# Optimization experiments

Measured on AMD Instinct MI355X. Metric: run time of the kernel, lower is better.

## Reference

```python
import jax, jax.numpy as jnp
import numpy as np

B, S, E, H, FF = 8, 1024, 1024, 16, 4096
DK = E // H
EPS = 1.1920929e-07  # torch RMSNorm default eps = finfo(float32).eps


def _rmsnorm(x, g):
    return x * jax.lax.rsqrt(jnp.mean(x * x, axis=-1, keepdims=True) + EPS) * g


def _rope(q, k):
    # q, k: [B, H, S, DK]; standard rotate-half RoPE, theta=10000
    d = q.shape[-1]
    s = q.shape[-2]
    inv_freq = 1.0 / (10000.0 ** (jnp.arange(0, d, 2, dtype=jnp.float32) / d))
    ang = jnp.arange(s, dtype=jnp.float32)[:, None] * inv_freq  # [S, d/2]
    cos = jnp.concatenate([jnp.cos(ang), jnp.cos(ang)], axis=-1)  # [S, d]
    sin = jnp.concatenate([jnp.sin(ang), jnp.sin(ang)], axis=-1)

    def rot(x):
        x1, x2 = jnp.split(x, 2, axis=-1)
        return jnp.concatenate([-x2, x1], axis=-1)

    return q * cos + rot(q) * sin, k * cos + rot(k) * sin


def setup_inputs() -> dict:
    key = jax.random.key(0)
    ks = jax.random.split(key, 16)
    sc = 0.02
    inp = {
        "x": jax.random.normal(ks[0], (B, S, E), dtype=jnp.float32),
        "WQ": jax.random.normal(ks[1], (E, E), dtype=jnp.float32) * sc,
        "bQ": jnp.zeros((E,), jnp.float32),
        "WK": jax.random.normal(ks[2], (E, E), dtype=jnp.float32) * sc,
        "bK": jnp.zeros((E,), jnp.float32),
        "WV": jax.random.normal(ks[3], (E, E), dtype=jnp.float32) * sc,
        "bV": jnp.zeros((E,), jnp.float32),
        "WO": jax.random.normal(ks[4], (E, E), dtype=jnp.float32) * sc,
        "bO": jnp.zeros((E,), jnp.float32),
        "W1": jax.random.normal(ks[5], (E, FF), dtype=jnp.float32) * sc,
        "b1": jnp.zeros((FF,), jnp.float32),
        "W2": jax.random.normal(ks[6], (FF, E), dtype=jnp.float32) * sc,
        "b2": jnp.zeros((E,), jnp.float32),
        "g1": jnp.ones((E,), jnp.float32),
        "g2": jnp.ones((E,), jnp.float32),
    }
    return inp


def reference(x, WQ, bQ, WK, bK, WV, bV, WO, bO, W1, b1, W2, b2, g1, g2):
    b, s, e = x.shape

    def attn(h):
        q = (h @ WQ + bQ).reshape(b, s, H, DK).transpose(0, 2, 1, 3)
        k = (h @ WK + bK).reshape(b, s, H, DK).transpose(0, 2, 1, 3)
        v = (h @ WV + bV).reshape(b, s, H, DK).transpose(0, 2, 1, 3)
        q, k = _rope(q, k)
        scores = jnp.einsum("bhqd,bhkd->bhqk", q, k) / jnp.sqrt(jnp.float32(DK))
        p = jax.nn.softmax(scores, axis=-1)
        o = jnp.einsum("bhqk,bhkd->bhqd", p, v)
        o = o.transpose(0, 2, 1, 3).reshape(b, s, e)
        return o @ WO + bO

    def ffn(h):
        return jax.nn.relu(h @ W1 + b1) @ W2 + b2

    x = x + attn(_rmsnorm(x, g1))
    x = x + ffn(_rmsnorm(x, g2))
    return x
```

## Files before the change

### kernel.cpp

```cpp
#include <hip/hip_runtime.h>
#include <math.h>

#define B_ 8
#define S_ 1024
#define E_ 1024
#define H_ 16
#define FF_ 4096

typedef __attribute__((ext_vector_type(8))) short bf16x8;
typedef __attribute__((ext_vector_type(4))) float f32x4;

__device__ __forceinline__ unsigned short f2bf(float f) {
  union { float f; unsigned u; } v;
  v.f = f;
  unsigned r = v.u + 0x7fffu + ((v.u >> 16) & 1u);
  return (unsigned short)(r >> 16);
}
__device__ __forceinline__ float bf2f(unsigned short u) {
  union { unsigned u; float f; } v;
  v.u = ((unsigned)u) << 16;
  return v.f;
}
__device__ __forceinline__ unsigned fbits(float f) {
  union { float f; unsigned u; } v;
  v.f = f;
  return v.u;
}

__device__ __forceinline__ void glds16(const void* g, void* l) {
  __builtin_amdgcn_global_load_lds(
      (const __attribute__((address_space(1))) unsigned int*)g,
      (__attribute__((address_space(3))) unsigned int*)l, 16, 0, 0);
}

__global__ __launch_bounds__(256) void wconvT(const float* __restrict__ W,
                                              unsigned short* __restrict__ Wt,
                                              int K, int N) {
  __shared__ float t[32][33];
  const int tx = threadIdx.x & 31, ty = threadIdx.x >> 5;
  const int n0 = blockIdx.x * 32, k0 = blockIdx.y * 32;
#pragma unroll
  for (int p = 0; p < 4; ++p)
    t[ty + p * 8][tx] = W[(size_t)(k0 + ty + p * 8) * N + n0 + tx];
  __syncthreads();
#pragma unroll
  for (int p = 0; p < 4; ++p)
    Wt[(size_t)(n0 + ty + p * 8) * K + k0 + tx] = f2bf(t[tx][ty + p * 8]);
}

__global__ __launch_bounds__(256) void bpack(const float* __restrict__ bQ,
                                             const float* __restrict__ bK,
                                             const float* __restrict__ bV,
                                             float* __restrict__ o) {
  const int i = blockIdx.x * 256 + threadIdx.x;
  const float v = (i < 1024) ? bQ[i] : ((i < 2048) ? bK[i - 1024] : bV[i - 2048]);
  o[i] = v;
}

__global__ __launch_bounds__(256) void rmsnorm_kernel(const float* __restrict__ x,
                                                      const float* __restrict__ g,
                                                      unsigned short* __restrict__ out) {
  const int row = blockIdx.x;
  const int t = threadIdx.x;
  const float4 v = ((const float4*)(x + (size_t)row * E_))[t];
  float ss = v.x * v.x + v.y * v.y + v.z * v.z + v.w * v.w;
#pragma unroll
  for (int off = 32; off > 0; off >>= 1) ss += __shfl_down(ss, off);
  __shared__ float sred[4];
  if ((t & 63) == 0) sred[t >> 6] = ss;
  __syncthreads();
  const float tot = sred[0] + sred[1] + sred[2] + sred[3];
  const float rinv = rsqrtf(tot * (1.0f / E_) + 1.1920929e-07f);
  const float4 gv = ((const float4*)g)[t];
  ushort4 o;
  o.x = f2bf(v.x * rinv * gv.x);
  o.y = f2bf(v.y * rinv * gv.y);
  o.z = f2bf(v.z * rinv * gv.z);
  o.w = f2bf(v.w * rinv * gv.w);
  ((ushort4*)(out + (size_t)row * E_))[t] = o;
}

template <int OUT_BF16, int RELU, int RES>
__global__ __launch_bounds__(256) void gemm_bf16(const unsigned short* __restrict__ A,
                                                 const unsigned short* __restrict__ Bt,
                                                 const float* __restrict__ bias,
                                                 const float* __restrict__ res,
                                                 void* __restrict__ C,
                                                 int M, int N, int K) {
  __shared__ unsigned short As[128 * 32];
  __shared__ unsigned short Bs[128 * 32];
  const int tid = threadIdx.x;
  const int w = tid >> 6;
  const int lane = tid & 63;

  const int nb = gridDim.x;
  const int id = blockIdx.x;
  const int lid = (id & 7) * (nb >> 3) + (id >> 3);
  const int per = (M >> 7) * 8;
  const int grp = lid / per;
  const int rem = lid - grp * per;
  const int bn = (grp * 8 + (rem & 7)) * 128;
  const int bm = (rem >> 3) * 128;

  const int wm = (w & 1) * 64, wn = (w >> 1) * 64;

  f32x4 acc[4][4];
#pragma unroll
  for (int i = 0; i < 4; ++i)
#pragma unroll
    for (int j = 0; j < 4; ++j) acc[i][j] = (f32x4){0.f, 0.f, 0.f, 0.f};

  const unsigned short* Ap0 = A + (size_t)(bm + w * 32 + (lane >> 2)) * K + (lane & 3) * 8;
  const unsigned short* Ap1 = Ap0 + (size_t)16 * K;
  const unsigned short* Bp0 = Bt + (size_t)(bn + w * 32 + (lane >> 2)) * K + (lane & 3) * 8;
  const unsigned short* Bp1 = Bp0 + (size_t)16 * K;
  unsigned short* AsD0 = &As[w * 1024];
  unsigned short* AsD1 = AsD0 + 512;
  unsigned short* BsD0 = &Bs[w * 1024];
  unsigned short* BsD1 = BsD0 + 512;

  const int fr = lane & 15;
  const int fk = (lane >> 4) * 8;

  for (int k0 = 0; k0 < K; k0 += 32) {
    __syncthreads();
    glds16(Ap0 + k0, AsD0);
    glds16(Ap1 + k0, AsD1);
    glds16(Bp0 + k0, BsD0);
    glds16(Bp1 + k0, BsD1);
    __syncthreads();
    bf16x8 a[4], b[4];
#pragma unroll
    for (int im = 0; im < 4; ++im)
      a[im] = *(const bf16x8*)&As[(wm + im * 16 + fr) * 32 + fk];
#pragma unroll
    for (int in = 0; in < 4; ++in)
      b[in] = *(const bf16x8*)&Bs[(wn + in * 16 + fr) * 32 + fk];
#pragma unroll
    for (int im = 0; im < 4; ++im)
#pragma unroll
      for (int in = 0; in < 4; ++in)
        acc[im][in] = __builtin_amdgcn_mfma_f32_16x16x32_bf16(a[im], b[in], acc[im][in], 0, 0, 0);
  }

#pragma unroll
  for (int im = 0; im < 4; ++im) {
    const int row0 = bm + wm + im * 16 + (lane >> 4) * 4;
#pragma unroll
    for (int in = 0; in < 4; ++in) {
      const int col = bn + wn + in * 16 + (lane & 15);
      const float bv = bias[col];
#pragma unroll
      for (int r = 0; r < 4; ++r) {
        float v = acc[im][in][r] + bv;
        if (RES) v += res[(size_t)(row0 + r) * N + col];
        if (RELU) v = fmaxf(v, 0.0f);
        if (OUT_BF16)
          ((unsigned short*)C)[(size_t)(row0 + r) * N + col] = f2bf(v);
        else
          ((float*)C)[(size_t)(row0 + r) * N + col] = v;
      }
    }
  }
}

#define QSCALE 0.1803368801111f
__global__ __launch_bounds__(256) void rope_kernel(unsigned short* __restrict__ QKV) {
  const int i = blockIdx.x * 256 + threadIdx.x;
  const int fi = i & 31;
  const int h = (i >> 5) & 15;
  const int bs = i >> 9;
  const int s = bs & (S_ - 1);
  const float inv = exp2f(-0.4152410118f * (float)fi);
  const float ang = (float)s * inv;
  const float cs = __cosf(ang), sn = __sinf(ang);
  const size_t base = (size_t)bs * 3072 + h * 64 + fi;
  const float q1 = bf2f(QKV[base]), q2 = bf2f(QKV[base + 32]);
  QKV[base] = f2bf((q1 * cs - q2 * sn) * QSCALE);
  QKV[base + 32] = f2bf((q2 * cs + q1 * sn) * QSCALE);
  const size_t kb = base + 1024;
  const float k1 = bf2f(QKV[kb]), k2 = bf2f(QKV[kb + 32]);
  QKV[kb] = f2bf(k1 * cs - k2 * sn);
  QKV[kb + 32] = f2bf(k2 * cs + k1 * sn);
}

__global__ __launch_bounds__(256) void vtrans(const unsigned short* __restrict__ QKV,
                                              unsigned short* __restrict__ Vt) {
  __shared__ unsigned short T[64 * 66];
  const int tid = threadIdx.x;
  const int st = blockIdx.x, bh = blockIdx.y;
  const int b = bh >> 4, h = bh & 15;
  const int sx = tid & 15, sy = tid >> 4;
#pragma unroll
  for (int p = 0; p < 4; ++p) {
    const int sl = p * 16 + sy;
    const ushort4 v = *(const ushort4*)&QKV[(size_t)(b * S_ + st * 64 + sl) * 3072 + 2048 + h * 64 + sx * 4];
    *(ushort4*)&T[sl * 66 + sx * 4] = v;
  }
  __syncthreads();
#pragma unroll
  for (int p = 0; p < 4; ++p) {
    const int dl = p * 16 + sy;
    ushort4 o;
    o.x = T[(sx * 4 + 0) * 66 + dl];
    o.y = T[(sx * 4 + 1) * 66 + dl];
    o.z = T[(sx * 4 + 2) * 66 + dl];
    o.w = T[(sx * 4 + 3) * 66 + dl];
    *(ushort4*)&Vt[(size_t)(bh * 64 + dl) * S_ + st * 64 + sx * 4] = o;
  }
}

__global__ __launch_bounds__(256) void attn_v3(const unsigned short* __restrict__ QKV,
                                               const unsigned short* __restrict__ Vt,
                                               unsigned short* __restrict__ Og) {
  __shared__ unsigned short Kf[8 * 512];
  __shared__ unsigned short Vf[8 * 512];
  __shared__ unsigned short Ps[4][32 * 72];
  const int tid = threadIdx.x;
  const int w = tid >> 6, lane = tid & 63;
  const int qt = blockIdx.x, bh = blockIdx.y;
  const int b = bh >> 4, h = bh & 15;
  const int fr = lane & 15, g = lane >> 4, fk = g * 8;
  const int q0w = qt * 128 + w * 32;

  bf16x8 qB[2][2];
#pragma unroll
  for (int nt = 0; nt < 2; ++nt)
#pragma unroll
    for (int c = 0; c < 2; ++c)
      qB[nt][c] = *(const bf16x8*)&QKV[(size_t)(b * S_ + q0w + nt * 16 + fr) * 3072 +
                                       h * 64 + c * 32 + fk];

  f32x4 o[4][2];
#pragma unroll
  for (int mt = 0; mt < 4; ++mt)
#pragma unroll
    for (int nt = 0; nt < 2; ++nt) o[mt][nt] = (f32x4){0.f, 0.f, 0.f, 0.f};
  float l[2] = {0.0f, 0.0f};

  for (int kt = 0; kt < 16; ++kt) {
    __syncthreads();
#pragma unroll
    for (int p = 0; p < 4; ++p) {
      const int u = w * 4 + p;
      if (u < 8) {
        const int mt = u >> 1, c = u & 1;
        glds16(QKV + (size_t)(b * S_ + kt * 64 + mt * 16 + fr) * 3072 +
                   1024 + h * 64 + c * 32 + fk,
               &Kf[u * 512]);
      } else {
        const int v = u - 8, mt = v >> 1, c = v & 1;
        glds16(Vt + (size_t)(bh * 64 + mt * 16 + fr) * S_ + kt * 64 + c * 32 + fk,
               &Vf[v * 512]);
      }
    }
    __syncthreads();

    f32x4 s[4][2];
#pragma unroll
    for (int mt = 0; mt < 4; ++mt) {
      const bf16x8 k0 = *(const bf16x8*)&Kf[(mt * 2 + 0) * 512 + lane * 8];
      const bf16x8 k1 = *(const bf16x8*)&Kf[(mt * 2 + 1) * 512 + lane * 8];
#pragma unroll
      for (int nt = 0; nt < 2; ++nt) {
        f32x4 a = (f32x4){0.f, 0.f, 0.f, 0.f};
        a = __builtin_amdgcn_mfma_f32_16x16x32_bf16(k0, qB[nt][0], a, 0, 0, 0);
        a = __builtin_amdgcn_mfma_f32_16x16x32_bf16(k1, qB[nt][1], a, 0, 0, 0);
        s[mt][nt] = a;
      }
    }

#pragma unroll
    for (int nt = 0; nt < 2; ++nt) {
      float rs = 0.0f;
#pragma unroll
      for (int mt = 0; mt < 4; ++mt)
#pragma unroll
        for (int r = 0; r < 4; ++r) {
          const float p = exp2f(s[mt][nt][r]);
          s[mt][nt][r] = p;
          rs += p;
        }
      rs += __shfl_xor(rs, 16);
      rs += __shfl_xor(rs, 32);
      l[nt] += rs;
    }

#pragma unroll
    for (int nt = 0; nt < 2; ++nt)
#pragma unroll
      for (int mt = 0; mt < 4; ++mt) {
        uint2 pk;
        pk.x = __builtin_amdgcn_perm(fbits(s[mt][nt][1]), fbits(s[mt][nt][0]), 0x07060302u);
        pk.y = __builtin_amdgcn_perm(fbits(s[mt][nt][3]), fbits(s[mt][nt][2]), 0x07060302u);
        *(uint2*)&Ps[w][(nt * 16 + fr) * 72 + mt * 16 + g * 4] = pk;
      }

    bf16x8 pB[2][2];
#pragma unroll
    for (int nt = 0; nt < 2; ++nt)
#pragma unroll
      for (int c = 0; c < 2; ++c)
        pB[nt][c] = *(const bf16x8*)&Ps[w][(nt * 16 + fr) * 72 + c * 32 + fk];
#pragma unroll
    for (int mt = 0; mt < 4; ++mt) {
      const bf16x8 v0 = *(const bf16x8*)&Vf[(mt * 2 + 0) * 512 + lane * 8];
      const bf16x8 v1 = *(const bf16x8*)&Vf[(mt * 2 + 1) * 512 + lane * 8];
#pragma unroll
      for (int nt = 0; nt < 2; ++nt) {
        o[mt][nt] = __builtin_amdgcn_mfma_f32_16x16x32_bf16(v0, pB[nt][0], o[mt][nt], 0, 0, 0);
        o[mt][nt] = __builtin_amdgcn_mfma_f32_16x16x32_bf16(v1, pB[nt][1], o[mt][nt], 0, 0, 0);
      }
    }
  }

  __syncthreads();
  const float linv0 = 1.0f / l[0], linv1 = 1.0f / l[1];
#pragma unroll
  for (int nt = 0; nt < 2; ++nt) {
    const float li = nt ? linv1 : linv0;
#pragma unroll
    for (int mt = 0; mt < 4; ++mt) {
      uint2 pk;
      pk.x = __builtin_amdgcn_perm(fbits(o[mt][nt][1] * li), fbits(o[mt][nt][0] * li), 0x07060302u);
      pk.y = __builtin_amdgcn_perm(fbits(o[mt][nt][3] * li), fbits(o[mt][nt][2] * li), 0x07060302u);
      *(uint2*)&Ps[w][(nt * 16 + fr) * 72 + mt * 16 + g * 4] = pk;
    }
  }
  __syncthreads();
  const int qr = lane >> 1, hf = lane & 1;
#pragma unroll
  for (int c = 0; c < 2; ++c) {
    const bf16x8 vv = *(const bf16x8*)&Ps[w][qr * 72 + hf * 16 + c * 32];
    *(bf16x8*)&Og[(size_t)(b * S_ + q0w + qr) * E_ + h * 64 + hf * 16 + c * 32] = vv;
  }
}

extern "C" void kernel_launch(void* const* d_in, const int* in_sizes, int n_in,
                              void* d_out, int out_size, void* d_ws, size_t ws_size,
                              hipStream_t stream) {
  const float* x  = (const float*)d_in[0];
  const float* WQ = (const float*)d_in[1];
  const float* bQ = (const float*)d_in[2];
  const float* WK = (const float*)d_in[3];
  const float* bK = (const float*)d_in[4];
  const float* WV = (const float*)d_in[5];
  const float* bV = (const float*)d_in[6];
  const float* WO = (const float*)d_in[7];
  const float* bO = (const float*)d_in[8];
  const float* W1 = (const float*)d_in[9];
  const float* b1 = (const float*)d_in[10];
  const float* W2 = (const float*)d_in[11];
  const float* b2 = (const float*)d_in[12];
  const float* g1 = (const float*)d_in[13];
  const float* g2 = (const float*)d_in[14];
  float* out = (float*)d_out;

  char* ws = (char*)d_ws;
  const size_t MB = 1024 * 1024;
  unsigned short* h1   = (unsigned short*)(ws + 0 * MB);
  unsigned short* QKV  = (unsigned short*)(ws + 16 * MB);
  unsigned short* Vt   = (unsigned short*)(ws + 64 * MB);
  unsigned short* Ob   = (unsigned short*)(ws + 80 * MB);
  float*          x1   = (float*)(ws + 96 * MB);
  unsigned short* h2   = (unsigned short*)(ws + 128 * MB);
  unsigned short* mid  = (unsigned short*)(ws + 16 * MB);
  unsigned short* WQKVt= (unsigned short*)(ws + 144 * MB);
  unsigned short* WOt  = (unsigned short*)(ws + 150 * MB);
  unsigned short* W1t  = (unsigned short*)(ws + 152 * MB);
  unsigned short* W2t  = (unsigned short*)(ws + 160 * MB);
  float*          bqkv = (float*)(ws + 168 * MB);

  const int M = B_ * S_;

  wconvT<<<dim3(32, 32), 256, 0, stream>>>(WQ, WQKVt, E_, E_);
  wconvT<<<dim3(32, 32), 256, 0, stream>>>(WK, WQKVt + 1024 * 1024, E_, E_);
  wconvT<<<dim3(32, 32), 256, 0, stream>>>(WV, WQKVt + 2 * 1024 * 1024, E_, E_);
  wconvT<<<dim3(32, 32), 256, 0, stream>>>(WO, WOt, E_, E_);
  wconvT<<<dim3(128, 32), 256, 0, stream>>>(W1, W1t, E_, FF_);
  wconvT<<<dim3(32, 128), 256, 0, stream>>>(W2, W2t, FF_, E_);
  bpack<<<12, 256, 0, stream>>>(bQ, bK, bV, bqkv);

  rmsnorm_kernel<<<M, 256, 0, stream>>>(x, g1, h1);

  gemm_bf16<1, 0, 0><<<24 * 64, 256, 0, stream>>>(h1, WQKVt, bqkv, nullptr, QKV, M, 3072, E_);

  rope_kernel<<<(B_ * S_ * H_ * 32) / 256, 256, 0, stream>>>(QKV);

  vtrans<<<dim3(16, 128), 256, 0, stream>>>(QKV, Vt);

  attn_v3<<<dim3(8, B_ * H_), 256, 0, stream>>>(QKV, Vt, Ob);

  gemm_bf16<0, 0, 1><<<8 * 64, 256, 0, stream>>>(Ob, WOt, bO, x, x1, M, E_, E_);

  rmsnorm_kernel<<<M, 256, 0, stream>>>(x1, g2, h2);

  gemm_bf16<1, 1, 0><<<32 * 64, 256, 0, stream>>>(h2, W1t, b1, nullptr, mid, M, FF_, E_);

  gemm_bf16<0, 0, 1><<<8 * 64, 256, 0, stream>>>(mid, W2t, b2, x1, out, M, E_, FF_);
}
```

Before: 549.9 us.

## Fuse RoPE and V transpose into QKV GEMM, double-buffer attention, use N64 GEMM

The QKV projection GEMM now applies RoPE and the Q scale in its epilogue and writes V already transposed. This removes the separate rope and vtrans kernels and their extra global round trips. Attention gets double-buffered K/V shared-memory staging so the next tile's loads overlap compute, and some syncs are removed. The N=1024 output GEMMs (WO, W2) switch to a 128x64 tile kernel that launches 1024 blocks, raising occupancy and CU coverage. The risks are strided scalar stores in the QKV epilogue and a possible shared-memory race now that the barriers are gone.

```diff
diff --git a/kernel.cpp b/kernel.cpp
--- a/kernel.cpp
+++ b/kernel.cpp
@@ -9,6 +9,9 @@
 
 typedef __attribute__((ext_vector_type(8))) short bf16x8;
 typedef __attribute__((ext_vector_type(4))) float f32x4;
+
+#define QSCALE 0.1803368801111f
+#define LG2_10K 0.4152410118f
 
 __device__ __forceinline__ unsigned short f2bf(float f) {
   union { float f; unsigned u; } v;
@@ -164,57 +167,202 @@
   }
 }
 
-#define QSCALE 0.1803368801111f
-__global__ __launch_bounds__(256) void rope_kernel(unsigned short* __restrict__ QKV) {
-  const int i = blockIdx.x * 256 + threadIdx.x;
-  const int fi = i & 31;
-  const int h = (i >> 5) & 15;
-  const int bs = i >> 9;
-  const int s = bs & (S_ - 1);
-  const float inv = exp2f(-0.4152410118f * (float)fi);
-  const float ang = (float)s * inv;
-  const float cs = __cosf(ang), sn = __sinf(ang);
-  const size_t base = (size_t)bs * 3072 + h * 64 + fi;
-  const float q1 = bf2f(QKV[base]), q2 = bf2f(QKV[base + 32]);
-  QKV[base] = f2bf((q1 * cs - q2 * sn) * QSCALE);
-  QKV[base + 32] = f2bf((q2 * cs + q1 * sn) * QSCALE);
-  const size_t kb = base + 1024;
-  const float k1 = bf2f(QKV[kb]), k2 = bf2f(QKV[kb + 32]);
-  QKV[kb] = f2bf(k1 * cs - k2 * sn);
-  QKV[kb + 32] = f2bf(k2 * cs + k1 * sn);
-}
-
-__global__ __launch_bounds__(256) void vtrans(const unsigned short* __restrict__ QKV,
-                                              unsigned short* __restrict__ Vt) {
-  __shared__ unsigned short T[64 * 66];
+template <int OUT_BF16, int RELU, int RES>
+__global__ __launch_bounds__(256) void gemm_n64(const unsigned short* __restrict__ A,
+                                                const unsigned short* __restrict__ Bt,
+                                                const float* __restrict__ bias,
+                                                const float* __restrict__ res,
+                                                void* __restrict__ C,
+                                                int M, int N, int K) {
+  __shared__ unsigned short As[128 * 32];
+  __shared__ unsigned short Bs[64 * 32];
   const int tid = threadIdx.x;
-  const int st = blockIdx.x, bh = blockIdx.y;
-  const int b = bh >> 4, h = bh & 15;
-  const int sx = tid & 15, sy = tid >> 4;
-#pragma unroll
-  for (int p = 0; p < 4; ++p) {
-    const int sl = p * 16 + sy;
-    const ushort4 v = *(const ushort4*)&QKV[(size_t)(b * S_ + st * 64 + sl) * 3072 + 2048 + h * 64 + sx * 4];
-    *(ushort4*)&T[sl * 66 + sx * 4] = v;
-  }
-  __syncthreads();
-#pragma unroll
-  for (int p = 0; p < 4; ++p) {
-    const int dl = p * 16 + sy;
-    ushort4 o;
-    o.x = T[(sx * 4 + 0) * 66 + dl];
-    o.y = T[(sx * 4 + 1) * 66 + dl];
-    o.z = T[(sx * 4 + 2) * 66 + dl];
-    o.w = T[(sx * 4 + 3) * 66 + dl];
-    *(ushort4*)&Vt[(size_t)(bh * 64 + dl) * S_ + st * 64 + sx * 4] = o;
-  }
-}
-
-__global__ __launch_bounds__(256) void attn_v3(const unsigned short* __restrict__ QKV,
+  const int w = tid >> 6;
+  const int lane = tid & 63;
+
+  const int nbn = N >> 6;
+  const int bm = (blockIdx.x / nbn) * 128;
+  const int bn = (blockIdx.x % nbn) * 64;
+
+  const int wm = (w & 1) * 64, wn = (w >> 1) * 32;
+
+  f32x4 acc[4][2];
+#pragma unroll
+  for (int i = 0; i < 4; ++i)
+#pragma unroll
+    for (int j = 0; j < 2; ++j) acc[i][j] = (f32x4){0.f, 0.f, 0.f, 0.f};
+
+  const unsigned short* Ap0 = A + (size_t)(bm + w * 32 + (lane >> 2)) * K + (lane & 3) * 8;
+  const unsigned short* Ap1 = Ap0 + (size_t)16 * K;
+  const unsigned short* Bp0 = Bt + (size_t)(bn + w * 16 + (lane >> 2)) * K + (lane & 3) * 8;
+  unsigned short* AsD0 = &As[w * 1024];
+  unsigned short* AsD1 = AsD0 + 512;
+  unsigned short* BsD0 = &Bs[w * 512];
+
+  const int fr = lane & 15;
+  const int fk = (lane >> 4) * 8;
+
+  for (int k0 = 0; k0 < K; k0 += 32) {
+    __syncthreads();
+    glds16(Ap0 + k0, AsD0);
+    glds16(Ap1 + k0, AsD1);
+    glds16(Bp0 + k0, BsD0);
+    __syncthreads();
+    bf16x8 a[4], b[2];
+#pragma unroll
+    for (int im = 0; im < 4; ++im)
+      a[im] = *(const bf16x8*)&As[(wm + im * 16 + fr) * 32 + fk];
+#pragma unroll
+    for (int in = 0; in < 2; ++in)
+      b[in] = *(const bf16x8*)&Bs[(wn + in * 16 + fr) * 32 + fk];
+#pragma unroll
+    for (int im = 0; im < 4; ++im)
+#pragma unroll
+      for (int in = 0; in < 2; ++in)
+        acc[im][in] = __builtin_amdgcn_mfma_f32_16x16x32_bf16(a[im], b[in], acc[im][in], 0, 0, 0);
+  }
+
+#pragma unroll
+  for (int im = 0; im < 4; ++im) {
+    const int row0 = bm + wm + im * 16 + (lane >> 4) * 4;
+#pragma unroll
+    for (int in = 0; in < 2; ++in) {
+      const int col = bn + wn + in * 16 + fr;
+      const float bv = bias[col];
+#pragma unroll
+      for (int r = 0; r < 4; ++r) {
+        float v = acc[im][in][r] + bv;
+        if (RES) v += res[(size_t)(row0 + r) * N + col];
+        if (RELU) v = fmaxf(v, 0.0f);
+        if (OUT_BF16)
+          ((unsigned short*)C)[(size_t)(row0 + r) * N + col] = f2bf(v);
+        else
+          ((float*)C)[(size_t)(row0 + r) * N + col] = v;
+      }
+    }
+  }
+}
+
+__global__ __launch_bounds__(256) void gemm_qkv(const unsigned short* __restrict__ A,
+                                                const unsigned short* __restrict__ Bt,
+                                                const float* __restrict__ bias,
+                                                unsigned short* __restrict__ QKV,
+                                                unsigned short* __restrict__ Vt,
+                                                int M, int K) {
+  const int N = 3072;
+  __shared__ unsigned short As[128 * 32];
+  __shared__ unsigned short Bs[128 * 32];
+  const int tid = threadIdx.x;
+  const int w = tid >> 6;
+  const int lane = tid & 63;
+
+  const int nb = gridDim.x;
+  const int id = blockIdx.x;
+  const int lid = (id & 7) * (nb >> 3) + (id >> 3);
+  const int per = (M >> 7) * 8;
+  const int grp = lid / per;
+  const int rem = lid - grp * per;
+  const int bn = (grp * 8 + (rem & 7)) * 128;
+  const int bm = (rem >> 3) * 128;
+
+  const int wm = (w & 1) * 64, wn = (w >> 1) * 64;
+
+  f32x4 acc[4][4];
+#pragma unroll
+  for (int i = 0; i < 4; ++i)
+#pragma unroll
+    for (int j = 0; j < 4; ++j) acc[i][j] = (f32x4){0.f, 0.f, 0.f, 0.f};
+
+  const unsigned short* Ap0 = A + (size_t)(bm + w * 32 + (lane >> 2)) * K + (lane & 3) * 8;
+  const unsigned short* Ap1 = Ap0 + (size_t)16 * K;
+  const unsigned short* Bp0 = Bt + (size_t)(bn + w * 32 + (lane >> 2)) * K + (lane & 3) * 8;
+  const unsigned short* Bp1 = Bp0 + (size_t)16 * K;
+  unsigned short* AsD0 = &As[w * 1024];
+  unsigned short* AsD1 = AsD0 + 512;
+  unsigned short* BsD0 = &Bs[w * 1024];
+  unsigned short* BsD1 = BsD0 + 512;
+
+  const int fr = lane & 15;
+  const int fk = (lane >> 4) * 8;
+
+  for (int k0 = 0; k0 < K; k0 += 32) {
+    __syncthreads();
+    glds16(Ap0 + k0, AsD0);
+    glds16(Ap1 + k0, AsD1);
+    glds16(Bp0 + k0, BsD0);
+    glds16(Bp1 + k0, BsD1);
+    __syncthreads();
+    bf16x8 a[4], b[4];
+#pragma unroll
+    for (int im = 0; im < 4; ++im)
+      a[im] = *(const bf16x8*)&As[(wm + im * 16 + fr) * 32 + fk];
+#pragma unroll
+    for (int in = 0; in < 4; ++in)
+      b[in] = *(const bf16x8*)&Bs[(wn + in * 16 + fr) * 32 + fk];
+#pragma unroll
+    for (int im = 0; im < 4; ++im)
+#pragma unroll
+      for (int in = 0; in < 4; ++in)
+        acc[im][in] = __builtin_amdgcn_mfma_f32_16x16x32_bf16(a[im], b[in], acc[im][in], 0, 0, 0);
+  }
+
+  const int cbase = bn + wn;
+  const int seg = cbase >> 6;
+  const int typ = seg >> 4;
+  const int hh = seg & 15;
+  const int bidx = bm >> 10;
+  float bv[4];
+#pragma unroll
+  for (int in = 0; in < 4; ++in) bv[in] = bias[cbase + in * 16 + fr];
+
+  if (typ == 2) {
+#pragma unroll
+    for (int im = 0; im < 4; ++im) {
+      const int s0 = (bm & 1023) + wm + im * 16 + (lane >> 4) * 4;
+#pragma unroll
+      for (int in = 0; in < 4; ++in) {
+        const int d = in * 16 + fr;
+        ushort4 o4;
+        o4.x = f2bf(acc[im][in][0] + bv[in]);
+        o4.y = f2bf(acc[im][in][1] + bv[in]);
+        o4.z = f2bf(acc[im][in][2] + bv[in]);
+        o4.w = f2bf(acc[im][in][3] + bv[in]);
+        *(ushort4*)&Vt[(size_t)((bidx * 16 + hh) * 64 + d) * S_ + s0] = o4;
+      }
+    }
+  } else {
+    const float qs = (typ == 0) ? QSCALE : 1.0f;
+    const float i0 = exp2f(-LG2_10K * (float)fr);
+    const float i1 = exp2f(-LG2_10K * (float)(fr + 16));
+#pragma unroll
+    for (int im = 0; im < 4; ++im) {
+      const int row0 = bm + wm + im * 16 + (lane >> 4) * 4;
+#pragma unroll
+      for (int r = 0; r < 4; ++r) {
+        const int row = row0 + r;
+        const float s = (float)(row & 1023);
+        float sn0, cs0, sn1, cs1;
+        __sincosf(s * i0, &sn0, &cs0);
+        __sincosf(s * i1, &sn1, &cs1);
+        const float x0 = acc[im][0][r] + bv[0];
+        const float x1 = acc[im][1][r] + bv[1];
+        const float x2 = acc[im][2][r] + bv[2];
+        const float x3 = acc[im][3][r] + bv[3];
+        unsigned short* cp = QKV + (size_t)row * 3072 + cbase;
+        cp[fr]      = f2bf((x0 * cs0 - x2 * sn0) * qs);
+        cp[16 + fr] = f2bf((x1 * cs1 - x3 * sn1) * qs);
+        cp[32 + fr] = f2bf((x2 * cs0 + x0 * sn0) * qs);
+        cp[48 + fr] = f2bf((x3 * cs1 + x1 * sn1) * qs);
+      }
+    }
+  }
+}
+
+__global__ __launch_bounds__(256) void attn_v4(const unsigned short* __restrict__ QKV,
                                                const unsigned short* __restrict__ Vt,
                                                unsigned short* __restrict__ Og) {
-  __shared__ unsigned short Kf[8 * 512];
-  __shared__ unsigned short Vf[8 * 512];
+  __shared__ unsigned short Kf[2][8 * 512];
+  __shared__ unsigned short Vf[2][8 * 512];
   __shared__ unsigned short Ps[4][32 * 72];
   const int tid = threadIdx.x;
   const int w = tid >> 6, lane = tid & 63;
@@ -238,29 +386,36 @@
     for (int nt = 0; nt < 2; ++nt) o[mt][nt] = (f32x4){0.f, 0.f, 0.f, 0.f};
   float l[2] = {0.0f, 0.0f};
 
+#define STAGE(kt, bufi)                                                                   \
+  {                                                                                       \
+    _Pragma("unroll") for (int p = 0; p < 4; ++p) {                                       \
+      const int u = w * 4 + p;                                                            \
+      if (u < 8) {                                                                        \
+        const int mt = u >> 1, c = u & 1;                                                 \
+        glds16(QKV + (size_t)(b * S_ + (kt) * 64 + mt * 16 + fr) * 3072 + 1024 + h * 64 + \
+                   c * 32 + fk,                                                           \
+               &Kf[bufi][u * 512]);                                                       \
+      } else {                                                                            \
+        const int v2 = u - 8, mt = v2 >> 1, c = v2 & 1;                                   \
+        glds16(Vt + (size_t)(bh * 64 + mt * 16 + fr) * S_ + (kt) * 64 + c * 32 + fk,      \
+               &Vf[bufi][v2 * 512]);                                                      \
+      }                                                                                   \
+    }                                                                                     \
+  }
+
+  STAGE(0, 0);
+
   for (int kt = 0; kt < 16; ++kt) {
     __syncthreads();
-#pragma unroll
-    for (int p = 0; p < 4; ++p) {
-      const int u = w * 4 + p;
-      if (u < 8) {
-        const int mt = u >> 1, c = u & 1;
-        glds16(QKV + (size_t)(b * S_ + kt * 64 + mt * 16 + fr) * 3072 +
-                   1024 + h * 64 + c * 32 + fk,
-               &Kf[u * 512]);
-      } else {
-        const int v = u - 8, mt = v >> 1, c = v & 1;
-        glds16(Vt + (size_t)(bh * 64 + mt * 16 + fr) * S_ + kt * 64 + c * 32 + fk,
-               &Vf[v * 512]);
-      }
-    }
-    __syncthreads();
+    if (kt < 15) STAGE(kt + 1, (kt + 1) & 1);
+    const unsigned short* Kc = Kf[kt & 1];
+    const unsigned short* Vc = Vf[kt & 1];
 
     f32x4 s[4][2];
 #pragma unroll
     for (int mt = 0; mt < 4; ++mt) {
-      const bf16x8 k0 = *(const bf16x8*)&Kf[(mt * 2 + 0) * 512 + lane * 8];
-      const bf16x8 k1 = *(const bf16x8*)&Kf[(mt * 2 + 1) * 512 + lane * 8];
+      const bf16x8 k0 = *(const bf16x8*)&Kc[(mt * 2 + 0) * 512 + lane * 8];
+      const bf16x8 k1 = *(const bf16x8*)&Kc[(mt * 2 + 1) * 512 + lane * 8];
 #pragma unroll
       for (int nt = 0; nt < 2; ++nt) {
         f32x4 a = (f32x4){0.f, 0.f, 0.f, 0.f};
@@ -304,8 +459,8 @@
         pB[nt][c] = *(const bf16x8*)&Ps[w][(nt * 16 + fr) * 72 + c * 32 + fk];
 #pragma unroll
     for (int mt = 0; mt < 4; ++mt) {
-      const bf16x8 v0 = *(const bf16x8*)&Vf[(mt * 2 + 0) * 512 + lane * 8];
-      const bf16x8 v1 = *(const bf16x8*)&Vf[(mt * 2 + 1) * 512 + lane * 8];
+      const bf16x8 v0 = *(const bf16x8*)&Vc[(mt * 2 + 0) * 512 + lane * 8];
+      const bf16x8 v1 = *(const bf16x8*)&Vc[(mt * 2 + 1) * 512 + lane * 8];
 #pragma unroll
       for (int nt = 0; nt < 2; ++nt) {
         o[mt][nt] = __builtin_amdgcn_mfma_f32_16x16x32_bf16(v0, pB[nt][0], o[mt][nt], 0, 0, 0);
@@ -314,7 +469,6 @@
     }
   }
 
-  __syncthreads();
   const float linv0 = 1.0f / l[0], linv1 = 1.0f / l[1];
 #pragma unroll
   for (int nt = 0; nt < 2; ++nt) {
@@ -327,7 +481,6 @@
       *(uint2*)&Ps[w][(nt * 16 + fr) * 72 + mt * 16 + g * 4] = pk;
     }
   }
-  __syncthreads();
   const int qr = lane >> 1, hf = lane & 1;
 #pragma unroll
   for (int c = 0; c < 2; ++c) {
@@ -383,19 +536,15 @@
 
   rmsnorm_kernel<<<M, 256, 0, stream>>>(x, g1, h1);
 
-  gemm_bf16<1, 0, 0><<<24 * 64, 256, 0, stream>>>(h1, WQKVt, bqkv, nullptr, QKV, M, 3072, E_);
-
-  rope_kernel<<<(B_ * S_ * H_ * 32) / 256, 256, 0, stream>>>(QKV);
-
-  vtrans<<<dim3(16, 128), 256, 0, stream>>>(QKV, Vt);
-
-  attn_v3<<<dim3(8, B_ * H_), 256, 0, stream>>>(QKV, Vt, Ob);
-
-  gemm_bf16<0, 0, 1><<<8 * 64, 256, 0, stream>>>(Ob, WOt, bO, x, x1, M, E_, E_);
+  gemm_qkv<<<24 * 64, 256, 0, stream>>>(h1, WQKVt, bqkv, QKV, Vt, M, E_);
+
+  attn_v4<<<dim3(8, B_ * H_), 256, 0, stream>>>(QKV, Vt, Ob);
+
+  gemm_n64<0, 0, 1><<<64 * 16, 256, 0, stream>>>(Ob, WOt, bO, x, x1, M, E_, E_);
 
   rmsnorm_kernel<<<M, 256, 0, stream>>>(x1, g2, h2);
 
   gemm_bf16<1, 1, 0><<<32 * 64, 256, 0, stream>>>(h2, W1t, b1, nullptr, mid, M, FF_, E_);
 
-  gemm_bf16<0, 0, 1><<<8 * 64, 256, 0, stream>>>(mid, W2t, b2, x1, out, M, E_, FF_);
-}
+  gemm_n64<0, 0, 1><<<64 * 16, 256, 0, stream>>>(mid, W2t, b2, x1, out, M, E_, FF_);
+}
```

Result: no change. 542.8 us (-1.3%).
